# Kernel optimization log

Hardware: AMD Instinct MI355X
Metric: run time of the kernel (lower is better)

The kernel has to match this reference:

```python
import jax, jax.numpy as jnp
import numpy as np

EPS = 1e-5

def _bn_relu(x, gamma, beta):
    # BatchNorm2d in training mode: biased batch stats over (B, H, W)
    mu = jnp.mean(x, axis=(0, 2, 3), keepdims=True)
    var = jnp.mean((x - mu) ** 2, axis=(0, 2, 3), keepdims=True)
    xh = (x - mu) * jax.lax.rsqrt(var + EPS)
    return jax.nn.relu(xh * gamma[None, :, None, None] + beta[None, :, None, None])

def setup_inputs() -> dict:
    key = jax.random.key(0)
    ks = jax.random.split(key, 16)
    B, N, D = 4, 256, 256            # in_channels = 2*D = 512
    feats = jax.random.normal(ks[0], (B, 1 + 2 * N, D), dtype=jnp.float32)
    def lin(k, o, c):
        return jax.random.normal(k, (o, c), dtype=jnp.float32) * (1.0 / np.sqrt(c))
    return {
        "feats": feats,
        "W1": lin(ks[1], 256, 512), "b1": jnp.zeros((256,), jnp.float32),
        "g1": jnp.ones((256,), jnp.float32), "be1": jnp.zeros((256,), jnp.float32),
        "W2": lin(ks[2], 128, 256), "b2": jnp.zeros((128,), jnp.float32),
        "g2": jnp.ones((128,), jnp.float32), "be2": jnp.zeros((128,), jnp.float32),
        "W3": lin(ks[3], 64, 128), "b3": jnp.zeros((64,), jnp.float32),
        "g3": jnp.ones((64,), jnp.float32), "be3": jnp.zeros((64,), jnp.float32),
        "W4": lin(ks[4], 1, 64), "b4": jnp.zeros((1,), jnp.float32),
    }

def reference(feats, W1, b1, g1, be1, W2, b2, g2, be2, W3, b3, g3, be3, W4, b4):
    B, T, Dfull = feats.shape
    f = feats[:, 1:]                                  # [B, 2N, D]
    N = f.shape[1] // 2
    D = f.shape[2]
    f = f.reshape(B, N, 2, D).mean(axis=2)            # [B, N, D]
    fc = jnp.transpose(f, (0, 2, 1))                  # [B, D, N]
    # conv1(cat(x, t)) fused: first D input channels see f_i, last D see f_j
    a = jnp.einsum('oc,bcn->bon', W1[:, :D], fc)      # [B, 256, N]
    bpart = jnp.einsum('oc,bcn->bon', W1[:, D:], fc)  # [B, 256, N]
    h = a[:, :, :, None] + bpart[:, :, None, :] + b1[None, :, None, None]  # [B,256,N,N]
    h = _bn_relu(h, g1, be1)
    h = jnp.einsum('oc,bcij->boij', W2, h) + b2[None, :, None, None]
    h = _bn_relu(h, g2, be2)
    h = jnp.einsum('oc,bcij->boij', W3, h) + b3[None, :, None, None]
    h = _bn_relu(h, g3, be3)
    h = jnp.einsum('oc,bcij->boij', W4, h) + b4[None, :, None, None]
    return h[:, 0]                                    # [B, N, N]
```

## Files before the change

### kernel.cpp

```cpp
#include <hip/hip_runtime.h>
#include <hip/hip_bf16.h>

#define EPS 1e-5f

typedef __attribute__((ext_vector_type(8))) short bf16x8;
typedef __attribute__((ext_vector_type(4))) float f32x4;

static constexpr size_t OFF_FT    = 0;
static constexpr size_t OFF_W1T   = 1048576;
static constexpr size_t OFF_W2B   = 1572864;
static constexpr size_t OFF_W3B   = 1638400;
static constexpr size_t OFF_S1    = 1654784;
static constexpr size_t OFF_T1    = 1655808;
static constexpr size_t OFF_STATS = 1656832;
static constexpr size_t OFF_S2    = 1658368;
static constexpr size_t OFF_T2    = 1658880;
static constexpr size_t OFF_S3    = 1659392;
static constexpr size_t OFF_T3    = 1659648;
static constexpr size_t OFF_ABT   = 1703936;
static constexpr size_t OFF_H2T   = 4194304;
static constexpr size_t OFF_H3T   = 71303168;

static __device__ inline float bfu2f(unsigned int u16) {
    return __uint_as_float(u16 << 16);
}
static __device__ inline unsigned short f2bfu(float f) {
    unsigned int u = __float_as_uint(f);
    unsigned int r = u + 0x7fffu + ((u >> 16) & 1u);
    return (unsigned short)(r >> 16);
}

static __device__ inline float blockReduce256(float v, float* sred) {
    #pragma unroll
    for (int off = 32; off > 0; off >>= 1) v += __shfl_down(v, off);
    int lane = threadIdx.x & 63, w = threadIdx.x >> 6;
    __syncthreads();
    if (lane == 0) sred[w] = v;
    __syncthreads();
    return sred[0] + sred[1] + sred[2] + sred[3];
}

__global__ void k0_pairmean_T(const float* __restrict__ feats, float* __restrict__ fT) {
    __shared__ float s[64][65];
    int b = blockIdx.x >> 2;
    int n0 = (blockIdx.x & 3) * 64;
    int tid = threadIdx.x;
    const float* fb = feats + (size_t)b * 513 * 256;
    for (int c0 = 0; c0 < 256; c0 += 64) {
        for (int idx = tid; idx < 64 * 64; idx += 256) {
            int n = idx >> 6, c = idx & 63;
            const float* r = fb + (size_t)(1 + 2 * (n0 + n)) * 256 + c0 + c;
            s[n][c] = 0.5f * (r[0] + r[256]);
        }
        __syncthreads();
        for (int idx = tid; idx < 64 * 64; idx += 256) {
            int c = idx >> 6, n = idx & 63;
            fT[((size_t)b * 256 + c0 + c) * 256 + n0 + n] = s[n][c];
        }
        __syncthreads();
    }
}

__global__ void kt_prep(const float* __restrict__ W1, const float* __restrict__ W2,
                        const float* __restrict__ W3, float* __restrict__ W1T,
                        unsigned short* __restrict__ W2b, unsigned short* __restrict__ W3b) {
    int idx = blockIdx.x * 256 + threadIdx.x;
    if (idx < 131072) {
        int c = idx >> 9, o = idx & 511;
        W1T[idx] = (o < 256) ? W1[(size_t)o * 512 + c] : W1[(size_t)(o - 256) * 512 + 256 + c];
    } else if (idx < 163840) {
        int j = idx - 131072;
        W2b[j] = f2bfu(W2[j]);
    } else if (idx < 172032) {
        int j = idx - 163840;
        W3b[j] = f2bfu(W3[j]);
    }
}

__global__ __launch_bounds__(256) void k1_gemm(const float* __restrict__ W1T,
                                               const float* __restrict__ fT,
                                               float* __restrict__ abT) {
    __shared__ float sW[64][68];
    __shared__ float sF[64][68];
    int tid = threadIdx.x;
    int b = blockIdx.x >> 2, n0 = (blockIdx.x & 3) * 64;
    int o0 = blockIdx.y * 64;
    int jq = tid & 15, og = tid >> 4;
    float acc[4][4] = {};
    for (int c0 = 0; c0 < 256; c0 += 64) {
        for (int idx = tid; idx < 64 * 64; idx += 256) {
            int c = idx >> 6, o = idx & 63;
            sW[c][o] = W1T[(size_t)(c0 + c) * 512 + o0 + o];
        }
        for (int idx = tid; idx < 64 * 64; idx += 256) {
            int c = idx >> 6, n = idx & 63;
            sF[c][n] = fT[((size_t)b * 256 + c0 + c) * 256 + n0 + n];
        }
        __syncthreads();
        #pragma unroll 8
        for (int c = 0; c < 64; ++c) {
            float4 rv = *(const float4*)&sF[c][jq * 4];
            float4 wv = *(const float4*)&sW[c][og * 4];
            float rr[4] = {rv.x, rv.y, rv.z, rv.w};
            float ww[4] = {wv.x, wv.y, wv.z, wv.w};
            #pragma unroll
            for (int m = 0; m < 4; ++m)
                #pragma unroll
                for (int w = 0; w < 4; ++w) acc[m][w] += ww[m] * rr[w];
        }
        __syncthreads();
    }
    for (int w = 0; w < 4; ++w) {
        int n = n0 + jq * 4 + w;
        float4 v = {acc[0][w], acc[1][w], acc[2][w], acc[3][w]};
        *(float4*)&abT[((size_t)(b * 256) + n) * 512 + o0 + og * 4] = v;
    }
}

__global__ void k1b_stats(const float* __restrict__ abT, const float* __restrict__ g1,
                          const float* __restrict__ be1, float* __restrict__ s1,
                          float* __restrict__ t1) {
    __shared__ float sred[4];
    int c = blockIdx.x, tid = threadIdx.x;
    float msum = 0.f, e2sum = 0.f;
    for (int b = 0; b < 4; ++b) {
        float va = abT[((size_t)(b * 256) + tid) * 512 + c];
        float vb = abT[((size_t)(b * 256) + tid) * 512 + 256 + c];
        float Sa = blockReduce256(va, sred);
        float Qa = blockReduce256(va * va, sred);
        float Sb = blockReduce256(vb, sred);
        float Qb = blockReduce256(vb * vb, sred);
        float ma = Sa * (1.f / 256.f), mb = Sb * (1.f / 256.f);
        msum += ma + mb;
        e2sum += Qa * (1.f / 256.f) + Qb * (1.f / 256.f) + 2.f * ma * mb;
    }
    if (tid == 0) {
        float m = msum * 0.25f, e2 = e2sum * 0.25f;
        float var = e2 - m * m;
        float s = g1[c] * rsqrtf(var + EPS);
        s1[c] = s;
        t1[c] = be1[c] - m * s;
    }
}

__global__ __launch_bounds__(256) void k2_mfma(const float* __restrict__ abT,
                                               const unsigned short* __restrict__ W2b,
                                               const float* __restrict__ s1,
                                               const float* __restrict__ t1,
                                               unsigned short* __restrict__ h2T) {
    __shared__ __align__(16) char smem[34816];
    float* aaS = (float*)smem;
    float* ssS = (float*)(smem + 1024);
    unsigned short* sW = (unsigned short*)(smem + 2048);
    unsigned short* sB = (unsigned short*)(smem + 12288);
    unsigned short* sT = (unsigned short*)smem;

    int tid = threadIdx.x;
    int j0 = blockIdx.x * 128, i = blockIdx.y, b = blockIdx.z;

    {
        float av = abT[((size_t)(b * 256 + i)) * 512 + tid];
        float s = s1[tid];
        aaS[tid] = fmaf(av, s, t1[tid]);
        ssS[tid] = s;
    }
    __syncthreads();

    int lane = tid & 63, wv = tid >> 6;
    int wr = wv >> 1, wc = wv & 1;
    int lo = lane & 15, khi = lane >> 4;

    f32x4 acc[4][4] = {};

    int jrow = tid >> 1, half = tid & 1;
    const float* bpRow = abT + ((size_t)(b * 256 + j0 + jrow)) * 512 + 256 + half * 16;
    const unsigned short* wRow = W2b + jrow * 256 + half * 16;
    int cb0 = half * 16;

    for (int c0 = 0; c0 < 256; c0 += 32) {
        {
            uint4 v0 = *(const uint4*)(wRow + c0);
            uint4 v1 = *(const uint4*)(wRow + c0 + 8);
            uint4* dst = (uint4*)(sW + jrow * 40 + half * 16);
            dst[0] = v0; dst[1] = v1;
        }
        {
            float4 f0 = *(const float4*)(bpRow + c0);
            float4 f1 = *(const float4*)(bpRow + c0 + 4);
            float4 f2 = *(const float4*)(bpRow + c0 + 8);
            float4 f3 = *(const float4*)(bpRow + c0 + 12);
            float vv[16] = {f0.x,f0.y,f0.z,f0.w, f1.x,f1.y,f1.z,f1.w,
                            f2.x,f2.y,f2.z,f2.w, f3.x,f3.y,f3.z,f3.w};
            int cb = c0 + cb0;
            unsigned int u[8];
            #pragma unroll
            for (int e = 0; e < 8; ++e) {
                int c = cb + 2 * e;
                float r0 = fmaxf(fmaf(vv[2 * e],     ssS[c],     aaS[c]),     0.f);
                float r1 = fmaxf(fmaf(vv[2 * e + 1], ssS[c + 1], aaS[c + 1]), 0.f);
                u[e] = (unsigned int)f2bfu(r0) | ((unsigned int)f2bfu(r1) << 16);
            }
            uint4* dst = (uint4*)(sB + jrow * 40 + half * 16);
            dst[0] = make_uint4(u[0], u[1], u[2], u[3]);
            dst[1] = make_uint4(u[4], u[5], u[6], u[7]);
        }
        __syncthreads();
        const unsigned short* aBase = sW + (wr * 64 + lo) * 40 + khi * 8;
        const unsigned short* bBase = sB + (wc * 64 + lo) * 40 + khi * 8;
        bf16x8 af[4], bfr[4];
        #pragma unroll
        for (int fm = 0; fm < 4; ++fm) af[fm] = *(const bf16x8*)(aBase + fm * 16 * 40);
        #pragma unroll
        for (int fn = 0; fn < 4; ++fn) bfr[fn] = *(const bf16x8*)(bBase + fn * 16 * 40);
        #pragma unroll
        for (int fm = 0; fm < 4; ++fm)
            #pragma unroll
            for (int fn = 0; fn < 4; ++fn)
                acc[fm][fn] = __builtin_amdgcn_mfma_f32_16x16x32_bf16(af[fm], bfr[fn], acc[fm][fn], 0, 0, 0);
        __syncthreads();
    }

    #pragma unroll
    for (int fm = 0; fm < 4; ++fm)
        #pragma unroll
        for (int fn = 0; fn < 4; ++fn) {
            int oq = wr * 64 + fm * 16 + khi * 4;
            int j  = wc * 64 + fn * 16 + lo;
            ushort4 pk;
            pk.x = f2bfu(acc[fm][fn][0]); pk.y = f2bfu(acc[fm][fn][1]);
            pk.z = f2bfu(acc[fm][fn][2]); pk.w = f2bfu(acc[fm][fn][3]);
            *(ushort4*)(sT + j * 136 + oq) = pk;
        }
    __syncthreads();
    size_t gbase = (((size_t)(b * 256 + i)) * 256 + j0 + jrow) * 128 + half * 64;
    #pragma unroll
    for (int e = 0; e < 8; ++e) {
        uint4 v = *(const uint4*)(sT + jrow * 136 + half * 64 + e * 8);
        *(uint4*)(h2T + gbase + e * 8) = v;
    }
}

__global__ void kstatsT(const unsigned short* __restrict__ h, float* __restrict__ sum,
                        float* __restrict__ sumsq, int C, int rowsPerBlock) {
    __shared__ float red[256][8];
    int tid = threadIdx.x;
    int G = C >> 3;
    int g = tid & (G - 1);
    int rl = tid / G;
    int rstep = 256 / G;
    float s[8] = {}, q[8] = {};
    size_t r0 = (size_t)blockIdx.x * rowsPerBlock;
    for (int r = rl; r < rowsPerBlock; r += rstep) {
        const unsigned short* p = h + (r0 + r) * C + g * 8;
        uint4 v = *(const uint4*)p;
        unsigned int w[4] = {v.x, v.y, v.z, v.w};
        #pragma unroll
        for (int k = 0; k < 4; ++k) {
            float f0 = bfu2f(w[k] & 0xffffu);
            float f1 = bfu2f(w[k] >> 16);
            s[2 * k] += f0; q[2 * k] += f0 * f0;
            s[2 * k + 1] += f1; q[2 * k + 1] += f1 * f1;
        }
    }
    #pragma unroll
    for (int e = 0; e < 8; ++e) red[tid][e] = s[e];
    __syncthreads();
    if (tid < C) {
        int gg = tid >> 3, e = tid & 7;
        float a = 0.f;
        for (int m = 0; m < rstep; ++m) a += red[gg + m * G][e];
        atomicAdd(&sum[tid], a);
    }
    __syncthreads();
    #pragma unroll
    for (int e = 0; e < 8; ++e) red[tid][e] = q[e];
    __syncthreads();
    if (tid < C) {
        int gg = tid >> 3, e = tid & 7;
        float a = 0.f;
        for (int m = 0; m < rstep; ++m) a += red[gg + m * G][e];
        atomicAdd(&sumsq[tid], a);
    }
}

__global__ void kbnparam(const float* __restrict__ sum, const float* __restrict__ sumsq,
                         const float* __restrict__ g, const float* __restrict__ be,
                         float* __restrict__ s, float* __restrict__ t, int C, float invc) {
    int o = threadIdx.x;
    if (o < C) {
        float mean = sum[o] * invc;
        float var = sumsq[o] * invc - mean * mean;
        float sc = g[o] * rsqrtf(var + EPS);
        s[o] = sc;
        t[o] = be[o] - mean * sc;
    }
}

__global__ __launch_bounds__(256) void k3_mfma(const unsigned short* __restrict__ h2T,
                                               const unsigned short* __restrict__ W3b,
                                               const float* __restrict__ s2,
                                               const float* __restrict__ t2,
                                               unsigned short* __restrict__ h3T) {
    __shared__ __align__(16) char smem[38912];
    float* s2S = (float*)smem;
    float* t2S = (float*)(smem + 512);
    unsigned short* sW3 = (unsigned short*)(smem + 1024);
    unsigned short* sB  = (unsigned short*)(smem + 18432);
    unsigned short* sT  = (unsigned short*)(smem + 1024);

    int tid = threadIdx.x;
    int i = blockIdx.x, b = blockIdx.y;
    if (tid < 128) { s2S[tid] = s2[tid]; t2S[tid] = t2[tid]; }
    {
        int o = tid >> 2, qd = tid & 3;
        #pragma unroll
        for (int e = 0; e < 4; ++e) {
            uint4 v = *(const uint4*)(W3b + o * 128 + qd * 32 + e * 8);
            *(uint4*)(sW3 + o * 136 + qd * 32 + e * 8) = v;
        }
    }
    __syncthreads();

    int lane = tid & 63, wv = tid >> 6;
    int lo = lane & 15, khi = lane >> 4;

    f32x4 acc[4][4] = {};
    const unsigned short* src = h2T + (((size_t)(b * 256 + i)) * 256 + tid) * 128;

    for (int c0 = 0; c0 < 128; c0 += 32) {
        #pragma unroll
        for (int e = 0; e < 4; ++e) {
            uint4 v = *(const uint4*)(src + c0 + e * 8);
            unsigned int w[4] = {v.x, v.y, v.z, v.w};
            unsigned int ou[4];
            #pragma unroll
            for (int k = 0; k < 4; ++k) {
                int c = c0 + e * 8 + 2 * k;
                float f0 = bfu2f(w[k] & 0xffffu);
                float f1 = bfu2f(w[k] >> 16);
                float r0 = fmaxf(fmaf(f0, s2S[c],     t2S[c]),     0.f);
                float r1 = fmaxf(fmaf(f1, s2S[c + 1], t2S[c + 1]), 0.f);
                ou[k] = (unsigned int)f2bfu(r0) | ((unsigned int)f2bfu(r1) << 16);
            }
            *(uint4*)(sB + tid * 40 + e * 8) = make_uint4(ou[0], ou[1], ou[2], ou[3]);
        }
        __syncthreads();
        bf16x8 af[4], bfr[4];
        #pragma unroll
        for (int fm = 0; fm < 4; ++fm)
            af[fm] = *(const bf16x8*)(sW3 + (fm * 16 + lo) * 136 + c0 + khi * 8);
        #pragma unroll
        for (int fn = 0; fn < 4; ++fn)
            bfr[fn] = *(const bf16x8*)(sB + (wv * 64 + fn * 16 + lo) * 40 + khi * 8);
        #pragma unroll
        for (int fm = 0; fm < 4; ++fm)
            #pragma unroll
            for (int fn = 0; fn < 4; ++fn)
                acc[fm][fn] = __builtin_amdgcn_mfma_f32_16x16x32_bf16(af[fm], bfr[fn], acc[fm][fn], 0, 0, 0);
        __syncthreads();
    }

    #pragma unroll
    for (int fm = 0; fm < 4; ++fm)
        #pragma unroll
        for (int fn = 0; fn < 4; ++fn) {
            int oq = fm * 16 + khi * 4;
            int j  = wv * 64 + fn * 16 + lo;
            ushort4 pk;
            pk.x = f2bfu(acc[fm][fn][0]); pk.y = f2bfu(acc[fm][fn][1]);
            pk.z = f2bfu(acc[fm][fn][2]); pk.w = f2bfu(acc[fm][fn][3]);
            *(ushort4*)(sT + j * 72 + oq) = pk;
        }
    __syncthreads();
    size_t gbase = (((size_t)(b * 256 + i)) * 256 + tid) * 64;
    #pragma unroll
    for (int e = 0; e < 8; ++e) {
        uint4 v = *(const uint4*)(sT + tid * 72 + e * 8);
        *(uint4*)(h3T + gbase + e * 8) = v;
    }
}

__global__ __launch_bounds__(256) void k4_final(const unsigned short* __restrict__ h3T,
                                                const float* __restrict__ W4,
                                                const float* __restrict__ s3,
                                                const float* __restrict__ t3,
                                                const float* __restrict__ b4,
                                                float* __restrict__ out) {
    __shared__ __align__(16) char smem[37632];
    float* wS = (float*)smem;
    float* sS = (float*)(smem + 256);
    float* tS = (float*)(smem + 512);
    unsigned short* sL = (unsigned short*)(smem + 768);
    int tid = threadIdx.x;
    int i = blockIdx.x, b = blockIdx.y;
    if (tid < 64) { wS[tid] = W4[tid]; sS[tid] = s3[tid]; tS[tid] = t3[tid]; }
    const unsigned short* src = h3T + ((size_t)(b * 256 + i)) * 256 * 64;
    #pragma unroll
    for (int e = 0; e < 8; ++e) {
        int f = tid + 256 * e;
        uint4 v = *(const uint4*)(src + f * 8);
        *(uint4*)(sL + (f >> 3) * 72 + (f & 7) * 8) = v;
    }
    __syncthreads();
    float acc = 0.f;
    #pragma unroll
    for (int e = 0; e < 8; ++e) {
        uint4 v = *(const uint4*)(sL + tid * 72 + e * 8);
        unsigned int w[4] = {v.x, v.y, v.z, v.w};
        #pragma unroll
        for (int k = 0; k < 4; ++k) {
            int c = e * 8 + 2 * k;
            float f0 = bfu2f(w[k] & 0xffffu);
            float f1 = bfu2f(w[k] >> 16);
            acc += wS[c] * fmaxf(fmaf(f0, sS[c], tS[c]), 0.f);
            acc += wS[c + 1] * fmaxf(fmaf(f1, sS[c + 1], tS[c + 1]), 0.f);
        }
    }
    out[((size_t)(b * 256 + i)) * 256 + tid] = acc + b4[0];
}

extern "C" void kernel_launch(void* const* d_in, const int* in_sizes, int n_in,
                              void* d_out, int out_size, void* d_ws, size_t ws_size,
                              hipStream_t stream) {
    const float* feats = (const float*)d_in[0];
    const float* W1  = (const float*)d_in[1];
    const float* g1  = (const float*)d_in[3];
    const float* be1 = (const float*)d_in[4];
    const float* W2  = (const float*)d_in[5];
    const float* g2  = (const float*)d_in[7];
    const float* be2 = (const float*)d_in[8];
    const float* W3  = (const float*)d_in[9];
    const float* g3  = (const float*)d_in[11];
    const float* be3 = (const float*)d_in[12];
    const float* W4  = (const float*)d_in[13];
    const float* b4  = (const float*)d_in[14];

    char* ws = (char*)d_ws;
    float* fT   = (float*)(ws + OFF_FT);
    float* W1T  = (float*)(ws + OFF_W1T);
    unsigned short* W2b = (unsigned short*)(ws + OFF_W2B);
    unsigned short* W3b = (unsigned short*)(ws + OFF_W3B);
    float* abT  = (float*)(ws + OFF_ABT);
    float* s1   = (float*)(ws + OFF_S1);
    float* t1   = (float*)(ws + OFF_T1);
    float* sum2   = (float*)(ws + OFF_STATS);
    float* sumsq2 = (float*)(ws + OFF_STATS + 512);
    float* sum3   = (float*)(ws + OFF_STATS + 1024);
    float* sumsq3 = (float*)(ws + OFF_STATS + 1280);
    float* s2 = (float*)(ws + OFF_S2);
    float* t2 = (float*)(ws + OFF_T2);
    float* s3 = (float*)(ws + OFF_S3);
    float* t3 = (float*)(ws + OFF_T3);
    unsigned short* h2T = (unsigned short*)(ws + OFF_H2T);
    unsigned short* h3T = (unsigned short*)(ws + OFF_H3T);
    float* out = (float*)d_out;

    hipMemsetAsync(ws + OFF_STATS, 0, 1536, stream);

    k0_pairmean_T<<<16, 256, 0, stream>>>(feats, fT);
    kt_prep<<<672, 256, 0, stream>>>(W1, W2, W3, W1T, W2b, W3b);
    k1_gemm<<<dim3(16, 8), 256, 0, stream>>>(W1T, fT, abT);
    k1b_stats<<<256, 256, 0, stream>>>(abT, g1, be1, s1, t1);
    k2_mfma<<<dim3(2, 256, 4), 256, 0, stream>>>(abT, W2b, s1, t1, h2T);
    kstatsT<<<512, 256, 0, stream>>>(h2T, sum2, sumsq2, 128, 512);
    kbnparam<<<1, 128, 0, stream>>>(sum2, sumsq2, g2, be2, s2, t2, 128, 1.f / 262144.f);
    k3_mfma<<<dim3(256, 4), 256, 0, stream>>>(h2T, W3b, s2, t2, h3T);
    kstatsT<<<512, 256, 0, stream>>>(h3T, sum3, sumsq3, 64, 512);
    kbnparam<<<1, 64, 0, stream>>>(sum3, sumsq3, g3, be3, s3, t3, 64, 1.f / 262144.f);
    k4_final<<<dim3(256, 4), 256, 0, stream>>>(h3T, W4, s3, t3, b4, out);
}
```

Measured before the change: 264.5 us.

## Fuse BatchNorm statistics into GEMM epilogues and drop separate stats passes

Per-channel sum and sum-of-squares are now computed in the epilogues of k1_gemm, k2_mfma and k3_mfma, using wave shuffles, shared atomics and global atomics spread over 8 slots. This removes the two kstatsT kernels that re-read the large bf16 h2T/h3T intermediates and replaces the slow per-channel k1b_stats with a small reduction. k2_mfma also moves to a 64-wide K tile with vectorized loads, and bf16 packing uses the hardware convert. The cost is extra epilogue work and atomic contention, and statistics are now taken from fp32 accumulators rather than bf16-rounded values.

```diff
diff --git a/kernel.cpp b/kernel.cpp
--- a/kernel.cpp
+++ b/kernel.cpp
@@ -12,13 +12,15 @@
 static constexpr size_t OFF_W3B   = 1638400;
 static constexpr size_t OFF_S1    = 1654784;
 static constexpr size_t OFF_T1    = 1655808;
-static constexpr size_t OFF_STATS = 1656832;
 static constexpr size_t OFF_S2    = 1658368;
 static constexpr size_t OFF_T2    = 1658880;
 static constexpr size_t OFF_S3    = 1659392;
 static constexpr size_t OFF_T3    = 1659648;
+static constexpr size_t OFF_ST2   = 1660928;
+static constexpr size_t OFF_ST3   = 1669120;
 static constexpr size_t OFF_ABT   = 1703936;
 static constexpr size_t OFF_H2T   = 4194304;
+static constexpr size_t OFF_P1    = OFF_H2T;
 static constexpr size_t OFF_H3T   = 71303168;
 
 static __device__ inline float bfu2f(unsigned int u16) {
@@ -29,15 +31,9 @@
     unsigned int r = u + 0x7fffu + ((u >> 16) & 1u);
     return (unsigned short)(r >> 16);
 }
-
-static __device__ inline float blockReduce256(float v, float* sred) {
-    #pragma unroll
-    for (int off = 32; off > 0; off >>= 1) v += __shfl_down(v, off);
-    int lane = threadIdx.x & 63, w = threadIdx.x >> 6;
-    __syncthreads();
-    if (lane == 0) sred[w] = v;
-    __syncthreads();
-    return sred[0] + sred[1] + sred[2] + sred[3];
+static __device__ inline unsigned int pkbf(float lo, float hi) {
+    __hip_bfloat162 p = __float22bfloat162_rn(make_float2(lo, hi));
+    return *reinterpret_cast<unsigned int*>(&p);
 }
 
 __global__ void k0_pairmean_T(const float* __restrict__ feats, float* __restrict__ fT) {
@@ -79,7 +75,8 @@
 
 __global__ __launch_bounds__(256) void k1_gemm(const float* __restrict__ W1T,
                                                const float* __restrict__ fT,
-                                               float* __restrict__ abT) {
+                                               float* __restrict__ abT,
+                                               float2* __restrict__ part) {
     __shared__ float sW[64][68];
     __shared__ float sF[64][68];
     int tid = threadIdx.x;
@@ -115,31 +112,45 @@
         float4 v = {acc[0][w], acc[1][w], acc[2][w], acc[3][w]};
         *(float4*)&abT[((size_t)(b * 256) + n) * 512 + o0 + og * 4] = v;
     }
-}
-
-__global__ void k1b_stats(const float* __restrict__ abT, const float* __restrict__ g1,
+    #pragma unroll
+    for (int m = 0; m < 4; ++m) {
+        float s = 0.f, q = 0.f;
+        #pragma unroll
+        for (int w = 0; w < 4; ++w) { float v = acc[m][w]; s += v; q += v * v; }
+        #pragma unroll
+        for (int off = 8; off; off >>= 1) { s += __shfl_down(s, off); q += __shfl_down(q, off); }
+        if (jq == 0) part[(size_t)blockIdx.x * 512 + o0 + og * 4 + m] = make_float2(s, q);
+    }
+}
+
+__global__ void k1b_stats(const float2* __restrict__ part, const float* __restrict__ g1,
                           const float* __restrict__ be1, float* __restrict__ s1,
                           float* __restrict__ t1) {
-    __shared__ float sred[4];
-    int c = blockIdx.x, tid = threadIdx.x;
-    float msum = 0.f, e2sum = 0.f;
+    __shared__ float Sl[4][512], Ql[4][512];
+    int o = threadIdx.x;
     for (int b = 0; b < 4; ++b) {
-        float va = abT[((size_t)(b * 256) + tid) * 512 + c];
-        float vb = abT[((size_t)(b * 256) + tid) * 512 + 256 + c];
-        float Sa = blockReduce256(va, sred);
-        float Qa = blockReduce256(va * va, sred);
-        float Sb = blockReduce256(vb, sred);
-        float Qb = blockReduce256(vb * vb, sred);
-        float ma = Sa * (1.f / 256.f), mb = Sb * (1.f / 256.f);
-        msum += ma + mb;
-        e2sum += Qa * (1.f / 256.f) + Qb * (1.f / 256.f) + 2.f * ma * mb;
-    }
-    if (tid == 0) {
+        float s = 0.f, q = 0.f;
+        #pragma unroll
+        for (int nt = 0; nt < 4; ++nt) {
+            float2 p = part[(size_t)(b * 4 + nt) * 512 + o];
+            s += p.x; q += p.y;
+        }
+        Sl[b][o] = s; Ql[b][o] = q;
+    }
+    __syncthreads();
+    if (o < 256) {
+        float msum = 0.f, e2sum = 0.f;
+        #pragma unroll
+        for (int b = 0; b < 4; ++b) {
+            float ma = Sl[b][o] * (1.f / 256.f), mb = Sl[b][o + 256] * (1.f / 256.f);
+            msum += ma + mb;
+            e2sum += Ql[b][o] * (1.f / 256.f) + Ql[b][o + 256] * (1.f / 256.f) + 2.f * ma * mb;
+        }
         float m = msum * 0.25f, e2 = e2sum * 0.25f;
         float var = e2 - m * m;
-        float s = g1[c] * rsqrtf(var + EPS);
-        s1[c] = s;
-        t1[c] = be1[c] - m * s;
+        float s = g1[o] * rsqrtf(var + EPS);
+        s1[o] = s;
+        t1[o] = be1[o] - m * s;
     }
 }
 
@@ -147,12 +158,16 @@
                                                const unsigned short* __restrict__ W2b,
                                                const float* __restrict__ s1,
                                                const float* __restrict__ t1,
-                                               unsigned short* __restrict__ h2T) {
-    __shared__ __align__(16) char smem[34816];
+                                               unsigned short* __restrict__ h2T,
+                                               float* __restrict__ gS2,
+                                               float* __restrict__ gQ2) {
+    __shared__ __align__(16) char smem[39936];
     float* aaS = (float*)smem;
     float* ssS = (float*)(smem + 1024);
     unsigned short* sW = (unsigned short*)(smem + 2048);
-    unsigned short* sB = (unsigned short*)(smem + 12288);
+    unsigned short* sB = (unsigned short*)(smem + 20480);
+    float* sS = (float*)(smem + 38912);
+    float* sQ = (float*)(smem + 39424);
     unsigned short* sT = (unsigned short*)smem;
 
     int tid = threadIdx.x;
@@ -164,6 +179,7 @@
         aaS[tid] = fmaf(av, s, t1[tid]);
         ssS[tid] = s;
     }
+    if (tid < 128) { sS[tid] = 0.f; sQ[tid] = 0.f; }
     __syncthreads();
 
     int lane = tid & 63, wv = tid >> 6;
@@ -171,54 +187,62 @@
     int lo = lane & 15, khi = lane >> 4;
 
     f32x4 acc[4][4] = {};
-
-    int jrow = tid >> 1, half = tid & 1;
-    const float* bpRow = abT + ((size_t)(b * 256 + j0 + jrow)) * 512 + 256 + half * 16;
-    const unsigned short* wRow = W2b + jrow * 256 + half * 16;
-    int cb0 = half * 16;
-
-    for (int c0 = 0; c0 < 256; c0 += 32) {
-        {
-            uint4 v0 = *(const uint4*)(wRow + c0);
-            uint4 v1 = *(const uint4*)(wRow + c0 + 8);
-            uint4* dst = (uint4*)(sW + jrow * 40 + half * 16);
-            dst[0] = v0; dst[1] = v1;
-        }
-        {
-            float4 f0 = *(const float4*)(bpRow + c0);
-            float4 f1 = *(const float4*)(bpRow + c0 + 4);
-            float4 f2 = *(const float4*)(bpRow + c0 + 8);
-            float4 f3 = *(const float4*)(bpRow + c0 + 12);
-            float vv[16] = {f0.x,f0.y,f0.z,f0.w, f1.x,f1.y,f1.z,f1.w,
-                            f2.x,f2.y,f2.z,f2.w, f3.x,f3.y,f3.z,f3.w};
-            int cb = c0 + cb0;
-            unsigned int u[8];
-            #pragma unroll
-            for (int e = 0; e < 8; ++e) {
-                int c = cb + 2 * e;
-                float r0 = fmaxf(fmaf(vv[2 * e],     ssS[c],     aaS[c]),     0.f);
-                float r1 = fmaxf(fmaf(vv[2 * e + 1], ssS[c + 1], aaS[c + 1]), 0.f);
-                u[e] = (unsigned int)f2bfu(r0) | ((unsigned int)f2bfu(r1) << 16);
+    const float* bpB = abT + ((size_t)(b * 256 + j0)) * 512 + 256;
+
+    for (int c0 = 0; c0 < 256; c0 += 64) {
+        #pragma unroll
+        for (int k = 0; k < 4; ++k) {
+            int f = tid + k * 256; int o = f >> 3, cs = f & 7;
+            uint4 v = *(const uint4*)(W2b + o * 256 + c0 + cs * 8);
+            *(uint4*)(sW + o * 72 + cs * 8) = v;
+        }
+        #pragma unroll
+        for (int k = 0; k < 8; ++k) {
+            int f = tid + k * 256; int j = f >> 4, cs = f & 15;
+            float4 bp = *(const float4*)(bpB + (size_t)j * 512 + c0 + cs * 4);
+            float4 a4 = *(const float4*)&aaS[c0 + cs * 4];
+            float4 s4 = *(const float4*)&ssS[c0 + cs * 4];
+            float r0 = fmaxf(fmaf(bp.x, s4.x, a4.x), 0.f);
+            float r1 = fmaxf(fmaf(bp.y, s4.y, a4.y), 0.f);
+            float r2 = fmaxf(fmaf(bp.z, s4.z, a4.z), 0.f);
+            float r3 = fmaxf(fmaf(bp.w, s4.w, a4.w), 0.f);
+            *(uint2*)(sB + j * 72 + cs * 4) = make_uint2(pkbf(r0, r1), pkbf(r2, r3));
+        }
+        __syncthreads();
+        const unsigned short* aB = sW + (wr * 64 + lo) * 72 + khi * 8;
+        const unsigned short* bB = sB + (wc * 64 + lo) * 72 + khi * 8;
+        #pragma unroll
+        for (int ks = 0; ks < 2; ++ks) {
+            bf16x8 af[4], bfr[4];
+            #pragma unroll
+            for (int fm = 0; fm < 4; ++fm) af[fm] = *(const bf16x8*)(aB + fm * 16 * 72 + ks * 32);
+            #pragma unroll
+            for (int fn = 0; fn < 4; ++fn) bfr[fn] = *(const bf16x8*)(bB + fn * 16 * 72 + ks * 32);
+            #pragma unroll
+            for (int fm = 0; fm < 4; ++fm)
+                #pragma unroll
+                for (int fn = 0; fn < 4; ++fn)
+                    acc[fm][fn] = __builtin_amdgcn_mfma_f32_16x16x32_bf16(af[fm], bfr[fn], acc[fm][fn], 0, 0, 0);
+        }
+        __syncthreads();
+    }
+
+    #pragma unroll
+    for (int fm = 0; fm < 4; ++fm)
+        #pragma unroll
+        for (int r = 0; r < 4; ++r) {
+            float s = 0.f, q = 0.f;
+            #pragma unroll
+            for (int fn = 0; fn < 4; ++fn) { float v = acc[fm][fn][r]; s += v; q += v * v; }
+            #pragma unroll
+            for (int off = 8; off; off >>= 1) { s += __shfl_down(s, off); q += __shfl_down(q, off); }
+            if (lo == 0) {
+                int o = wr * 64 + fm * 16 + khi * 4 + r;
+                atomicAdd(&sS[o], s);
+                atomicAdd(&sQ[o], q);
             }
-            uint4* dst = (uint4*)(sB + jrow * 40 + half * 16);
-            dst[0] = make_uint4(u[0], u[1], u[2], u[3]);
-            dst[1] = make_uint4(u[4], u[5], u[6], u[7]);
-        }
-        __syncthreads();
-        const unsigned short* aBase = sW + (wr * 64 + lo) * 40 + khi * 8;
-        const unsigned short* bBase = sB + (wc * 64 + lo) * 40 + khi * 8;
-        bf16x8 af[4], bfr[4];
-        #pragma unroll
-        for (int fm = 0; fm < 4; ++fm) af[fm] = *(const bf16x8*)(aBase + fm * 16 * 40);
-        #pragma unroll
-        for (int fn = 0; fn < 4; ++fn) bfr[fn] = *(const bf16x8*)(bBase + fn * 16 * 40);
-        #pragma unroll
-        for (int fm = 0; fm < 4; ++fm)
-            #pragma unroll
-            for (int fn = 0; fn < 4; ++fn)
-                acc[fm][fn] = __builtin_amdgcn_mfma_f32_16x16x32_bf16(af[fm], bfr[fn], acc[fm][fn], 0, 0, 0);
-        __syncthreads();
-    }
+        }
+    __syncthreads();
 
     #pragma unroll
     for (int fm = 0; fm < 4; ++fm)
@@ -226,70 +250,37 @@
         for (int fn = 0; fn < 4; ++fn) {
             int oq = wr * 64 + fm * 16 + khi * 4;
             int j  = wc * 64 + fn * 16 + lo;
-            ushort4 pk;
-            pk.x = f2bfu(acc[fm][fn][0]); pk.y = f2bfu(acc[fm][fn][1]);
-            pk.z = f2bfu(acc[fm][fn][2]); pk.w = f2bfu(acc[fm][fn][3]);
-            *(ushort4*)(sT + j * 136 + oq) = pk;
-        }
-    __syncthreads();
-    size_t gbase = (((size_t)(b * 256 + i)) * 256 + j0 + jrow) * 128 + half * 64;
-    #pragma unroll
-    for (int e = 0; e < 8; ++e) {
-        uint4 v = *(const uint4*)(sT + jrow * 136 + half * 64 + e * 8);
-        *(uint4*)(h2T + gbase + e * 8) = v;
-    }
-}
-
-__global__ void kstatsT(const unsigned short* __restrict__ h, float* __restrict__ sum,
-                        float* __restrict__ sumsq, int C, int rowsPerBlock) {
-    __shared__ float red[256][8];
-    int tid = threadIdx.x;
-    int G = C >> 3;
-    int g = tid & (G - 1);
-    int rl = tid / G;
-    int rstep = 256 / G;
-    float s[8] = {}, q[8] = {};
-    size_t r0 = (size_t)blockIdx.x * rowsPerBlock;
-    for (int r = rl; r < rowsPerBlock; r += rstep) {
-        const unsigned short* p = h + (r0 + r) * C + g * 8;
-        uint4 v = *(const uint4*)p;
-        unsigned int w[4] = {v.x, v.y, v.z, v.w};
-        #pragma unroll
-        for (int k = 0; k < 4; ++k) {
-            float f0 = bfu2f(w[k] & 0xffffu);
-            float f1 = bfu2f(w[k] >> 16);
-            s[2 * k] += f0; q[2 * k] += f0 * f0;
-            s[2 * k + 1] += f1; q[2 * k + 1] += f1 * f1;
-        }
-    }
-    #pragma unroll
-    for (int e = 0; e < 8; ++e) red[tid][e] = s[e];
-    __syncthreads();
-    if (tid < C) {
-        int gg = tid >> 3, e = tid & 7;
-        float a = 0.f;
-        for (int m = 0; m < rstep; ++m) a += red[gg + m * G][e];
-        atomicAdd(&sum[tid], a);
-    }
-    __syncthreads();
-    #pragma unroll
-    for (int e = 0; e < 8; ++e) red[tid][e] = q[e];
-    __syncthreads();
-    if (tid < C) {
-        int gg = tid >> 3, e = tid & 7;
-        float a = 0.f;
-        for (int m = 0; m < rstep; ++m) a += red[gg + m * G][e];
-        atomicAdd(&sumsq[tid], a);
-    }
-}
-
-__global__ void kbnparam(const float* __restrict__ sum, const float* __restrict__ sumsq,
+            unsigned int u0 = pkbf(acc[fm][fn][0], acc[fm][fn][1]);
+            unsigned int u1 = pkbf(acc[fm][fn][2], acc[fm][fn][3]);
+            *(uint2*)(sT + j * 136 + oq) = make_uint2(u0, u1);
+        }
+    __syncthreads();
+    {
+        int jrow = tid >> 1, half = tid & 1;
+        size_t gbase = (((size_t)(b * 256 + i)) * 256 + j0 + jrow) * 128 + half * 64;
+        #pragma unroll
+        for (int e = 0; e < 8; ++e) {
+            uint4 v = *(const uint4*)(sT + jrow * 136 + half * 64 + e * 8);
+            *(uint4*)(h2T + gbase + e * 8) = v;
+        }
+    }
+    if (tid < 128) {
+        int slot = (i & 7) * 128;
+        atomicAdd(&gS2[slot + tid], sS[tid]);
+        atomicAdd(&gQ2[slot + tid], sQ[tid]);
+    }
+}
+
+__global__ void kbnparam(const float* __restrict__ gS, const float* __restrict__ gQ,
                          const float* __restrict__ g, const float* __restrict__ be,
                          float* __restrict__ s, float* __restrict__ t, int C, float invc) {
     int o = threadIdx.x;
     if (o < C) {
-        float mean = sum[o] * invc;
-        float var = sumsq[o] * invc - mean * mean;
+        float su = 0.f, qu = 0.f;
+        #pragma unroll
+        for (int k = 0; k < 8; ++k) { su += gS[k * C + o]; qu += gQ[k * C + o]; }
+        float mean = su * invc;
+        float var = qu * invc - mean * mean;
         float sc = g[o] * rsqrtf(var + EPS);
         s[o] = sc;
         t[o] = be[o] - mean * sc;
@@ -300,17 +291,22 @@
                                                const unsigned short* __restrict__ W3b,
                                                const float* __restrict__ s2,
                                                const float* __restrict__ t2,
-                                               unsigned short* __restrict__ h3T) {
-    __shared__ __align__(16) char smem[38912];
+                                               unsigned short* __restrict__ h3T,
+                                               float* __restrict__ gS3,
+                                               float* __restrict__ gQ3) {
+    __shared__ __align__(16) char smem[39424];
     float* s2S = (float*)smem;
     float* t2S = (float*)(smem + 512);
     unsigned short* sW3 = (unsigned short*)(smem + 1024);
     unsigned short* sB  = (unsigned short*)(smem + 18432);
+    float* sS = (float*)(smem + 38912);
+    float* sQ = (float*)(smem + 39168);
     unsigned short* sT  = (unsigned short*)(smem + 1024);
 
     int tid = threadIdx.x;
     int i = blockIdx.x, b = blockIdx.y;
     if (tid < 128) { s2S[tid] = s2[tid]; t2S[tid] = t2[tid]; }
+    if (tid < 64) { sS[tid] = 0.f; sQ[tid] = 0.f; }
     {
         int o = tid >> 2, qd = tid & 3;
         #pragma unroll
@@ -331,18 +327,21 @@
         #pragma unroll
         for (int e = 0; e < 4; ++e) {
             uint4 v = *(const uint4*)(src + c0 + e * 8);
-            unsigned int w[4] = {v.x, v.y, v.z, v.w};
-            unsigned int ou[4];
-            #pragma unroll
-            for (int k = 0; k < 4; ++k) {
-                int c = c0 + e * 8 + 2 * k;
-                float f0 = bfu2f(w[k] & 0xffffu);
-                float f1 = bfu2f(w[k] >> 16);
-                float r0 = fmaxf(fmaf(f0, s2S[c],     t2S[c]),     0.f);
-                float r1 = fmaxf(fmaf(f1, s2S[c + 1], t2S[c + 1]), 0.f);
-                ou[k] = (unsigned int)f2bfu(r0) | ((unsigned int)f2bfu(r1) << 16);
-            }
-            *(uint4*)(sB + tid * 40 + e * 8) = make_uint4(ou[0], ou[1], ou[2], ou[3]);
+            int c = c0 + e * 8;
+            float4 sa = *(const float4*)&s2S[c];
+            float4 sb = *(const float4*)&s2S[c + 4];
+            float4 ta = *(const float4*)&t2S[c];
+            float4 tb = *(const float4*)&t2S[c + 4];
+            float r0 = fmaxf(fmaf(bfu2f(v.x & 0xffffu), sa.x, ta.x), 0.f);
+            float r1 = fmaxf(fmaf(bfu2f(v.x >> 16),     sa.y, ta.y), 0.f);
+            float r2 = fmaxf(fmaf(bfu2f(v.y & 0xffffu), sa.z, ta.z), 0.f);
+            float r3 = fmaxf(fmaf(bfu2f(v.y >> 16),     sa.w, ta.w), 0.f);
+            float r4 = fmaxf(fmaf(bfu2f(v.z & 0xffffu), sb.x, tb.x), 0.f);
+            float r5 = fmaxf(fmaf(bfu2f(v.z >> 16),     sb.y, tb.y), 0.f);
+            float r6 = fmaxf(fmaf(bfu2f(v.w & 0xffffu), sb.z, tb.z), 0.f);
+            float r7 = fmaxf(fmaf(bfu2f(v.w >> 16),     sb.w, tb.w), 0.f);
+            *(uint4*)(sB + tid * 40 + e * 8) =
+                make_uint4(pkbf(r0, r1), pkbf(r2, r3), pkbf(r4, r5), pkbf(r6, r7));
         }
         __syncthreads();
         bf16x8 af[4], bfr[4];
@@ -359,6 +358,23 @@
                 acc[fm][fn] = __builtin_amdgcn_mfma_f32_16x16x32_bf16(af[fm], bfr[fn], acc[fm][fn], 0, 0, 0);
         __syncthreads();
     }
+
+    #pragma unroll
+    for (int fm = 0; fm < 4; ++fm)
+        #pragma unroll
+        for (int r = 0; r < 4; ++r) {
+            float s = 0.f, q = 0.f;
+            #pragma unroll
+            for (int fn = 0; fn < 4; ++fn) { float v = acc[fm][fn][r]; s += v; q += v * v; }
+            #pragma unroll
+            for (int off = 8; off; off >>= 1) { s += __shfl_down(s, off); q += __shfl_down(q, off); }
+            if (lo == 0) {
+                int o = fm * 16 + khi * 4 + r;
+                atomicAdd(&sS[o], s);
+                atomicAdd(&sQ[o], q);
+            }
+        }
+    __syncthreads();
 
     #pragma unroll
     for (int fm = 0; fm < 4; ++fm)
@@ -366,17 +382,23 @@
         for (int fn = 0; fn < 4; ++fn) {
             int oq = fm * 16 + khi * 4;
             int j  = wv * 64 + fn * 16 + lo;
-            ushort4 pk;
-            pk.x = f2bfu(acc[fm][fn][0]); pk.y = f2bfu(acc[fm][fn][1]);
-            pk.z = f2bfu(acc[fm][fn][2]); pk.w = f2bfu(acc[fm][fn][3]);
-            *(ushort4*)(sT + j * 72 + oq) = pk;
-        }
-    __syncthreads();
-    size_t gbase = (((size_t)(b * 256 + i)) * 256 + tid) * 64;
-    #pragma unroll
-    for (int e = 0; e < 8; ++e) {
-        uint4 v = *(const uint4*)(sT + tid * 72 + e * 8);
-        *(uint4*)(h3T + gbase + e * 8) = v;
+            unsigned int u0 = pkbf(acc[fm][fn][0], acc[fm][fn][1]);
+            unsigned int u1 = pkbf(acc[fm][fn][2], acc[fm][fn][3]);
+            *(uint2*)(sT + j * 72 + oq) = make_uint2(u0, u1);
+        }
+    __syncthreads();
+    {
+        size_t gbase = (((size_t)(b * 256 + i)) * 256 + tid) * 64;
+        #pragma unroll
+        for (int e = 0; e < 8; ++e) {
+            uint4 v = *(const uint4*)(sT + tid * 72 + e * 8);
+            *(uint4*)(h3T + gbase + e * 8) = v;
+        }
+    }
+    if (tid < 64) {
+        int slot = (i & 7) * 64;
+        atomicAdd(&gS3[slot + tid], sS[tid]);
+        atomicAdd(&gQ3[slot + tid], sQ[tid]);
     }
 }
 
@@ -443,29 +465,28 @@
     float* abT  = (float*)(ws + OFF_ABT);
     float* s1   = (float*)(ws + OFF_S1);
     float* t1   = (float*)(ws + OFF_T1);
-    float* sum2   = (float*)(ws + OFF_STATS);
-    float* sumsq2 = (float*)(ws + OFF_STATS + 512);
-    float* sum3   = (float*)(ws + OFF_STATS + 1024);
-    float* sumsq3 = (float*)(ws + OFF_STATS + 1280);
+    float* gS2  = (float*)(ws + OFF_ST2);
+    float* gQ2  = (float*)(ws + OFF_ST2 + 4096);
+    float* gS3  = (float*)(ws + OFF_ST3);
+    float* gQ3  = (float*)(ws + OFF_ST3 + 2048);
     float* s2 = (float*)(ws + OFF_S2);
     float* t2 = (float*)(ws + OFF_T2);
     float* s3 = (float*)(ws + OFF_S3);
     float* t3 = (float*)(ws + OFF_T3);
+    float2* part = (float2*)(ws + OFF_P1);
     unsigned short* h2T = (unsigned short*)(ws + OFF_H2T);
     unsigned short* h3T = (unsigned short*)(ws + OFF_H3T);
     float* out = (float*)d_out;
 
-    hipMemsetAsync(ws + OFF_STATS, 0, 1536, stream);
+    hipMemsetAsync(ws + OFF_ST2, 0, 12288, stream);
 
     k0_pairmean_T<<<16, 256, 0, stream>>>(feats, fT);
     kt_prep<<<672, 256, 0, stream>>>(W1, W2, W3, W1T, W2b, W3b);
-    k1_gemm<<<dim3(16, 8), 256, 0, stream>>>(W1T, fT, abT);
-    k1b_stats<<<256, 256, 0, stream>>>(abT, g1, be1, s1, t1);
-    k2_mfma<<<dim3(2, 256, 4), 256, 0, stream>>>(abT, W2b, s1, t1, h2T);
-    kstatsT<<<512, 256, 0, stream>>>(h2T, sum2, sumsq2, 128, 512);
-    kbnparam<<<1, 128, 0, stream>>>(sum2, sumsq2, g2, be2, s2, t2, 128, 1.f / 262144.f);
-    k3_mfma<<<dim3(256, 4), 256, 0, stream>>>(h2T, W3b, s2, t2, h3T);
-    kstatsT<<<512, 256, 0, stream>>>(h3T, sum3, sumsq3, 64, 512);
-    kbnparam<<<1, 64, 0, stream>>>(sum3, sumsq3, g3, be3, s3, t3, 64, 1.f / 262144.f);
+    k1_gemm<<<dim3(16, 8), 256, 0, stream>>>(W1T, fT, abT, part);
+    k1b_stats<<<1, 512, 0, stream>>>(part, g1, be1, s1, t1);
+    k2_mfma<<<dim3(2, 256, 4), 256, 0, stream>>>(abT, W2b, s1, t1, h2T, gS2, gQ2);
+    kbnparam<<<1, 128, 0, stream>>>(gS2, gQ2, g2, be2, s2, t2, 128, 1.f / 262144.f);
+    k3_mfma<<<dim3(256, 4), 256, 0, stream>>>(h2T, W3b, s2, t2, h3T, gS3, gQ3);
+    kbnparam<<<1, 64, 0, stream>>>(gS3, gQ3, g3, be3, s3, t3, 64, 1.f / 262144.f);
     k4_final<<<dim3(256, 4), 256, 0, stream>>>(h3T, W4, s3, t3, b4, out);
 }
```

Result: faster. 241.6 us (-8.7%).
